# Performance work log

Hardware: AMD Instinct MI355X
Metric: run time of the kernel (lower is better)

The kernel has to match this reference:

```python
import jax, jax.numpy as jnp
import numpy as np

EMB, HEADS, DEPTH, SEQ, BATCH = 256, 8, 4, 8192, 4
DH = EMB // HEADS  # 32
FF = 4 * EMB
EPS = 1e-5


def setup_inputs() -> dict:
    key = jax.random.key(0)
    ks = jax.random.split(key, 8)
    w = lambda k, shape: jax.random.normal(k, shape, dtype=jnp.float32) * 0.02
    D = DEPTH
    return {
        "x": jax.random.normal(ks[0], (BATCH, SEQ, EMB), dtype=jnp.float32),
        "Wq": w(ks[1], (D, EMB, EMB)),
        "Wk": w(ks[2], (D, EMB, EMB)),
        "Wv": w(ks[3], (D, EMB, EMB)),
        "Wo": w(ks[4], (D, EMB, EMB)),
        "bo": jnp.zeros((D, EMB), jnp.float32),
        "ln1_g": jnp.ones((D, EMB), jnp.float32),
        "ln1_b": jnp.zeros((D, EMB), jnp.float32),
        "W1": w(ks[5], (D, EMB, FF)),
        "b1": jnp.zeros((D, FF), jnp.float32),
        "W2": w(ks[6], (D, FF, EMB)),
        "b2": jnp.zeros((D, EMB), jnp.float32),
        "ln2_g": jnp.ones((D, EMB), jnp.float32),
        "ln2_b": jnp.zeros((D, EMB), jnp.float32),
    }


def _layernorm(x, g, b):
    mu = x.mean(-1, keepdims=True)
    var = ((x - mu) ** 2).mean(-1, keepdims=True)
    return (x - mu) * jax.lax.rsqrt(var + EPS) * g + b


def _linear_attn(x, Wq, Wk, Wv, Wo, bo):
    # lucidrains linear_attn: q,k scaled by d**-0.25; softmax q over feature dim,
    # k over sequence dim; context = k^T v (per head), out = q @ context.
    b, n, dm = x.shape
    split = lambda t: t.reshape(b, n, HEADS, DH).transpose(0, 2, 1, 3)  # -> bhnd
    scale = DH ** -0.25
    q = jax.nn.softmax(split(x @ Wq) * scale, axis=-1)   # over d
    k = jax.nn.softmax(split(x @ Wk) * scale, axis=-2)   # over n
    v = split(x @ Wv)
    context = jnp.einsum('bhnd,bhne->bhde', k, v)        # [b,h,d,d]
    out = jnp.einsum('bhnd,bhde->bhne', q, context)      # [b,h,n,d]
    out = out.transpose(0, 2, 1, 3).reshape(b, n, dm)
    return out @ Wo + bo


def _forward(x, Wq, Wk, Wv, Wo, bo, ln1_g, ln1_b, W1, b1, W2, b2, ln2_g, ln2_b):
    for i in range(DEPTH):
        h = _layernorm(x, ln1_g[i], ln1_b[i])
        x = x + _linear_attn(h, Wq[i], Wk[i], Wv[i], Wo[i], bo[i])
        h = _layernorm(x, ln2_g[i], ln2_b[i])
        x = x + (jax.nn.gelu(h @ W1[i] + b1[i], approximate=False) @ W2[i] + b2[i])
    return x


def reference(x, Wq, Wk, Wv, Wo, bo, ln1_g, ln1_b, W1, b1, W2, b2, ln2_g, ln2_b):
    return _forward(x, Wq, Wk, Wv, Wo, bo, ln1_g, ln1_b, W1, b1, W2, b2, ln2_g, ln2_b)
```

## Files before the change

kernel.cpp:

```cpp
#include <hip/hip_runtime.h>
#include <hip/hip_bf16.h>

typedef __attribute__((ext_vector_type(8))) short bf16x8;
typedef __attribute__((ext_vector_type(4))) float f32x4;

#define EMB 256
#define HEADS 8
#define DH 32
#define SEQ 8192
#define BATCH 4
#define NROWS (SEQ*BATCH)
#define FFD 1024
#define DEPTH 4
#define QKVN 768
#define SCALE 0.42044820762685725f
#define NCHUNK 128
#define ROWS_PER_CHUNK (SEQ/NCHUNK)

static __device__ __forceinline__ float bf2f(ushort u){
  union { unsigned int i; float f; } x; x.i = ((unsigned int)u) << 16; return x.f;
}
static __device__ __forceinline__ ushort f2bf(float f){
  union { __hip_bfloat16 h; ushort u; } cv;
  cv.h = __float2bfloat16(f);
  return cv.u;
}
static __device__ __forceinline__ float gelu_f(float v){
  float y = 0.7978845608028654f * (v + 0.044715f*v*v*v);
  float e = __expf(2.0f*y);
  return 0.5f*v*(1.0f + (1.0f - 2.0f/(e + 1.0f)));
}

static __device__ __forceinline__ void gload_lds16(const ushort* g, ushort* l){
  __builtin_amdgcn_global_load_lds(
      (const __attribute__((address_space(1))) unsigned int*)(uintptr_t)g,
      (__attribute__((address_space(3))) unsigned int*)(uintptr_t)l,
      16, 0, 0);
}

__global__ __launch_bounds__(256) void prep_weights(
    const float* __restrict__ Wq, const float* __restrict__ Wk,
    const float* __restrict__ Wv, const float* __restrict__ Wo,
    const float* __restrict__ W1, const float* __restrict__ W2,
    ushort* __restrict__ wqkv_t, ushort* __restrict__ wo_t,
    ushort* __restrict__ w1_t, ushort* __restrict__ w2_t)
{
  __shared__ float tile[32][33];
  int bid = blockIdx.x;
  int L = bid / 768, r = bid % 768;
  const float* src; ushort* dst; int K, N, tidx;
  if (r < 192){ int which = r >> 6; tidx = r & 63;
    src = (which==0?Wq:which==1?Wk:Wv) + (long)L*65536;
    dst = wqkv_t + (long)L*QKVN*EMB + which*EMB*EMB; K=256; N=256;
  } else if (r < 256){ tidx = r-192; src = Wo + (long)L*65536; dst = wo_t + (long)L*65536; K=256; N=256; }
  else if (r < 512){ tidx = r-256; src = W1 + (long)L*262144; dst = w1_t + (long)L*262144; K=256; N=1024; }
  else { tidx = r-512; src = W2 + (long)L*262144; dst = w2_t + (long)L*262144; K=1024; N=256; }
  int tn = N >> 5;
  int tk = tidx / tn, tj = tidx % tn;
  int k0 = tk*32, n0 = tj*32;
  int c = threadIdx.x & 31, r0 = threadIdx.x >> 5;
  #pragma unroll
  for (int i=0;i<4;i++){
    int rr = r0 + i*8;
    tile[rr][c] = src[(long)(k0+rr)*N + n0 + c];
  }
  __syncthreads();
  #pragma unroll
  for (int i=0;i<4;i++){
    int rr = r0 + i*8;
    dst[(long)(n0+rr)*K + k0 + c] = f2bf(tile[c][rr]);
  }
}

__global__ __launch_bounds__(256) void ln_kernel(const float* __restrict__ x,
    const float* __restrict__ g, const float* __restrict__ bb,
    ushort* __restrict__ h)
{
  int wid = threadIdx.x >> 6, lane = threadIdx.x & 63;
  long row = (long)blockIdx.x*4 + wid;
  const float4 xv = *(const float4*)(x + row*EMB + lane*4);
  float s = xv.x+xv.y+xv.z+xv.w;
  float s2 = xv.x*xv.x+xv.y*xv.y+xv.z*xv.z+xv.w*xv.w;
  #pragma unroll
  for (int m=1;m<64;m<<=1){ s += __shfl_xor(s,m,64); s2 += __shfl_xor(s2,m,64); }
  float mean = s * (1.0f/EMB);
  float inv = rsqrtf(s2*(1.0f/EMB) - mean*mean + 1e-5f);
  float4 gv = *(const float4*)(g + lane*4);
  float4 bv = *(const float4*)(bb + lane*4);
  ushort4 o;
  o.x = f2bf((xv.x-mean)*inv*gv.x + bv.x);
  o.y = f2bf((xv.y-mean)*inv*gv.y + bv.y);
  o.z = f2bf((xv.z-mean)*inv*gv.z + bv.z);
  o.w = f2bf((xv.w-mean)*inv*gv.w + bv.w);
  *(ushort4*)(h + row*EMB + lane*4) = o;
}

template<int MODE, int BM, int BN, int BK>
__global__ __launch_bounds__(512, 2) void gemm_bt(
    const ushort* __restrict__ A, const ushort* __restrict__ Bt,
    int M, int N, int K,
    const float* __restrict__ bias,
    const float* __restrict__ xinf, const ushort* __restrict__ xinb,
    float* __restrict__ xoutf, ushort* __restrict__ xoutb,
    ushort* __restrict__ outb,
    const float* __restrict__ lng, const float* __restrict__ lnb)
{
  constexpr int NF = BN/64;
  constexpr int MR = BM/32;
  constexpr int MH = MR/4;
  constexpr int KK = BK/32;
  constexpr int CPR = BK/8;
  constexpr int AI = BM*BK/4096;
  constexpr int BI = BN*BK/4096;
  constexpr int TI = AI + BI;
  constexpr int NPH = KK*MH;
  __shared__ ushort LDSraw[2*BM*BK + 2*BN*BK];
  ushort* Abuf0 = LDSraw;
  ushort* Abuf1 = LDSraw + BM*BK;
  ushort* Bbuf0 = LDSraw + 2*BM*BK;
  ushort* Bbuf1 = LDSraw + 2*BM*BK + BN*BK;
  int t = threadIdx.x;
  int lane = t & 63, wid = t >> 6;
  int wr = wid >> 2, wc = wid & 3;
  int wrb = wr*(BM/2), wcb = wc*(BN/4);
  long rowA0 = (long)blockIdx.x * BM;
  long colB0 = (long)blockIdx.y * BN;
  const ushort* gA[AI]; int dA[AI];
  #pragma unroll
  for (int i=0;i<AI;i++){
    int l = i*512 + t;
    int row = l / CPR;
    int clog = (t % CPR) ^ (row & (CPR-1));
    gA[i] = A + (rowA0 + row)*(long)K + clog*8;
    dA[i] = l*8;
  }
  const ushort* gB[BI]; int dB[BI];
  #pragma unroll
  for (int i=0;i<BI;i++){
    int l = i*512 + t;
    int row = l / CPR;
    int clog = (t % CPR) ^ (row & (CPR-1));
    gB[i] = Bt + (colB0 + row)*(long)K + clog*8;
    dB[i] = l*8;
  }
  ushort* Ac = Abuf0; ushort* An = Abuf1;
  ushort* Bc = Bbuf0; ushort* Bn = Bbuf1;
  f32x4 acc[MR][NF] = {};
  int fr = lane & 15, cr4 = lane >> 4;
  int nsteps = K / BK;
  #pragma unroll
  for (int i=0;i<AI;i++) gload_lds16(gA[i], Ac + dA[i]);
  #pragma unroll
  for (int i=0;i<BI;i++) gload_lds16(gB[i], Bc + dB[i]);
  asm volatile("s_waitcnt vmcnt(0)" ::: "memory");
  __syncthreads();
  for (int s = 0; s < nsteps; ++s){
    bool pf = (s+1 < nsteps);
    long knext = (long)(s+1) * BK;
    #pragma unroll
    for (int kk=0; kk<KK; ++kk){
      int chunk = (((kk*4 + cr4)) ^ (fr & (CPR-1))) << 3;
      bf16x8 bv[NF];
      #pragma unroll
      for (int n=0;n<NF;n++)
        bv[n] = *(const bf16x8*)(Bc + (wcb + n*16 + fr)*BK + chunk);
      #pragma unroll
      for (int mh=0; mh<MH; ++mh){
        int sp = kk*MH + mh;
        bf16x8 av[4];
        #pragma unroll
        for (int m=0;m<4;m++)
          av[m] = *(const bf16x8*)(Ac + (wrb + (mh*4+m)*16 + fr)*BK + chunk);
        if (pf){
          #pragma unroll
          for (int j=0;j<TI;j++){
            if (j*NPH >= sp*TI && j*NPH < (sp+1)*TI){
              if (j < AI) gload_lds16(gA[j]+knext, An+dA[j]);
              else        gload_lds16(gB[j-AI]+knext, Bn+dB[j-AI]);
            }
          }
        }
        __builtin_amdgcn_s_setprio(1);
        #pragma unroll
        for (int m=0;m<4;m++){
          #pragma unroll
          for (int n=0;n<NF;n++)
            acc[mh*4+m][n] = __builtin_amdgcn_mfma_f32_16x16x32_bf16(av[m], bv[n], acc[mh*4+m][n], 0,0,0);
        }
        __builtin_amdgcn_s_setprio(0);
      }
    }
    asm volatile("s_waitcnt vmcnt(0)" ::: "memory");
    __syncthreads();
    ushort* tp;
    tp = Ac; Ac = An; An = tp;
    tp = Bc; Bc = Bn; Bn = tp;
  }
  constexpr int BNP = BN + 4;
  constexpr int ROUNDS = BM/32;
  constexpr int RPH = BM/64;
  float* bounce = (float*)LDSraw;
  int fq = lane >> 4;
  constexpr int TPR = BN/4;
  int rdrow = t / TPR;
  int rdcol = (t % TPR) * 4;
  constexpr int RPP = 512 / TPR;
  constexpr int PASSES = 32 / RPP;
  #pragma unroll
  for (int r = 0; r < ROUNDS; ++r){
    __syncthreads();
    if (wr == r / RPH){
      int mb = (r % RPH)*2;
      #pragma unroll
      for (int m4=0;m4<2;m4++){
        #pragma unroll
        for (int n=0;n<NF;n++){
          #pragma unroll
          for (int i=0;i<4;i++)
            bounce[(m4*16 + fq*4 + i)*BNP + wcb + n*16 + fr] = acc[mb+m4][n][i];
        }
      }
    }
    __syncthreads();
    long gr0 = rowA0 + r*32;
    #pragma unroll
    for (int p=0;p<PASSES;p++){
      int lr = p*RPP + rdrow;
      long gr = gr0 + lr;
      long gc = colB0 + rdcol;
      float4 v = *(float4*)&bounce[lr*BNP + rdcol];
      if (MODE==0){
        ushort4 o; o.x=f2bf(v.x); o.y=f2bf(v.y); o.z=f2bf(v.z); o.w=f2bf(v.w);
        *(ushort4*)&outb[gr*N + gc] = o;
      } else if (MODE==2){
        const float4 bv4 = *(const float4*)&bias[gc];
        ushort4 o;
        o.x = f2bf(gelu_f(v.x + bv4.x)); o.y = f2bf(gelu_f(v.y + bv4.y));
        o.z = f2bf(gelu_f(v.z + bv4.z)); o.w = f2bf(gelu_f(v.w + bv4.w));
        *(ushort4*)&outb[gr*N + gc] = o;
      } else {
        const float4 bv4 = *(const float4*)&bias[gc];
        float xo0, xo1, xo2, xo3;
        if (MODE==3){
          const float4 xo = *(const float4*)&xinf[gr*N + gc];
          xo0=xo.x; xo1=xo.y; xo2=xo.z; xo3=xo.w;
        } else {
          const ushort4 xb = *(const ushort4*)&xinb[gr*N + gc];
          xo0=bf2f(xb.x); xo1=bf2f(xb.y); xo2=bf2f(xb.z); xo3=bf2f(xb.w);
        }
        v.x += bv4.x + xo0; v.y += bv4.y + xo1;
        v.z += bv4.z + xo2; v.w += bv4.w + xo3;
        if (MODE==5){
          *(float4*)&xoutf[gr*N + gc] = v;
        } else {
          ushort4 xw;
          xw.x=f2bf(v.x); xw.y=f2bf(v.y); xw.z=f2bf(v.z); xw.w=f2bf(v.w);
          *(ushort4*)&xoutb[gr*N + gc] = xw;
          float s1 = v.x+v.y+v.z+v.w;
          float s2 = v.x*v.x+v.y*v.y+v.z*v.z+v.w*v.w;
          #pragma unroll
          for (int mm=1;mm<64;mm<<=1){ s1 += __shfl_xor(s1,mm,64); s2 += __shfl_xor(s2,mm,64); }
          float mean = s1 * (1.0f/EMB);
          float inv = rsqrtf(s2*(1.0f/EMB) - mean*mean + 1e-5f);
          const float4 g4 = *(const float4*)&lng[gc];
          const float4 b4 = *(const float4*)&lnb[gc];
          ushort4 o;
          o.x = f2bf((v.x-mean)*inv*g4.x + b4.x);
          o.y = f2bf((v.y-mean)*inv*g4.y + b4.y);
          o.z = f2bf((v.z-mean)*inv*g4.z + b4.z);
          o.w = f2bf((v.w-mean)*inv*g4.w + b4.w);
          *(ushort4*)&outb[gr*EMB + gc] = o;
        }
      }
    }
  }
}

__global__ __launch_bounds__(256) void colstats_partial(const ushort* __restrict__ qkv,
    float* __restrict__ pmax, float* __restrict__ psum)
{
  int ch = blockIdx.x, b = blockIdx.y;
  int t = threadIdx.x;
  const ushort* base = qkv + ((long)b*SEQ + (long)ch*ROWS_PER_CHUNK)*QKVN + EMB + t;
  float m[4] = {-1e30f,-1e30f,-1e30f,-1e30f};
  float s[4] = {0.f,0.f,0.f,0.f};
  #pragma unroll 2
  for (int n = 0; n < ROWS_PER_CHUNK; n += 4){
    #pragma unroll
    for (int j=0;j<4;j++){
      float v = bf2f(base[(long)(n+j)*QKVN]) * SCALE;
      float m2 = fmaxf(m[j], v);
      s[j] = s[j]*__expf(m[j]-m2) + __expf(v-m2);
      m[j] = m2;
    }
  }
  float M = fmaxf(fmaxf(m[0],m[1]), fmaxf(m[2],m[3]));
  float S = s[0]*__expf(m[0]-M) + s[1]*__expf(m[1]-M)
          + s[2]*__expf(m[2]-M) + s[3]*__expf(m[3]-M);
  long idx = ((long)b*NCHUNK + ch)*EMB + t;
  pmax[idx] = M; psum[idx] = S;
}

__global__ __launch_bounds__(256) void colstats_reduce(const float* __restrict__ pmax,
    const float* __restrict__ psum, float* __restrict__ kmax, float* __restrict__ ksum)
{
  int b = blockIdx.x, t = threadIdx.x;
  const float* pm = pmax + (long)b*NCHUNK*EMB + t;
  const float* ps = psum + (long)b*NCHUNK*EMB + t;
  float m = -1e30f, s = 0.f;
  for (int c = 0; c < NCHUNK; ++c){
    float cm = pm[(long)c*EMB], cs = ps[(long)c*EMB];
    float m2 = fmaxf(m, cm);
    s = s*__expf(m-m2) + cs*__expf(cm-m2);
    m = m2;
  }
  kmax[b*EMB + t] = m;
  ksum[b*EMB + t] = s;
}

__global__ __launch_bounds__(256) void ctx_partial(
    const ushort* __restrict__ qkv, const float* __restrict__ kmax,
    float* __restrict__ ctx_part)
{
  constexpr int LT = 72;
  __shared__ ushort ekT[32*LT];
  __shared__ ushort vvT[32*LT];
  int ch = blockIdx.x, h = blockIdx.y, b = blockIdx.z;
  int t = threadIdx.x, lane = t & 63, wid = t >> 6;
  long nbase = (long)b*SEQ + ch*512;
  int lrow = t >> 2, lseg = (t & 3) << 3;
  float km[8];
  #pragma unroll
  for (int j=0;j<8;j++) km[j] = kmax[b*256 + h*DH + lseg + j];
  int wstep = wid & 1, wdr = (wid >> 1) << 4;
  f32x4 acc0 = {}, acc1 = {};
  int frow = lane & 15, g8 = (lane >> 4) << 3;
  for (int st = 0; st < 8; ++st){
    long n0 = nbase + st*64;
    const ushort* gk = qkv + (n0 + lrow)*QKVN + EMB + h*DH + lseg;
    uint4 kv = *(const uint4*)gk;
    uint4 vv = *(const uint4*)(gk + EMB);
    __syncthreads();
    const ushort* kp = (const ushort*)&kv;
    const ushort* vp = (const ushort*)&vv;
    #pragma unroll
    for (int j=0;j<8;j++){
      float f = bf2f(kp[j])*SCALE;
      ekT[(lseg+j)*LT + lrow] = f2bf(__expf(f - km[j]));
      vvT[(lseg+j)*LT + lrow] = vp[j];
    }
    __syncthreads();
    bf16x8 afr = *(const bf16x8*)(ekT + (wdr + frow)*LT + wstep*32 + g8);
    bf16x8 bf0 = *(const bf16x8*)(vvT + frow*LT + wstep*32 + g8);
    bf16x8 bf1 = *(const bf16x8*)(vvT + (16 + frow)*LT + wstep*32 + g8);
    acc0 = __builtin_amdgcn_mfma_f32_16x16x32_bf16(afr, bf0, acc0, 0,0,0);
    acc1 = __builtin_amdgcn_mfma_f32_16x16x32_bf16(afr, bf1, acc1, 0,0,0);
  }
  int fq = lane >> 4;
  long pb = (((long)(b*HEADS+h))*32 + (ch*2+wstep))*1024;
  #pragma unroll
  for (int i=0;i<4;i++){
    ctx_part[pb + (wdr + fq*4 + i)*32 + frow] = acc0[i];
    ctx_part[pb + (wdr + fq*4 + i)*32 + 16 + frow] = acc1[i];
  }
}

__global__ __launch_bounds__(256) void ctx_reduce(const float* __restrict__ ctx_part,
    const float* __restrict__ ksum, ushort* __restrict__ ctxT)
{
  int bh = blockIdx.x; int b = bh >> 3, h = bh & 7;
  int t = threadIdx.x; int d = t >> 3, e4 = (t & 7) << 2;
  const float* p = ctx_part + (long)bh*32768 + d*32 + e4;
  float sx=0, sy=0, sz=0, sw=0;
  for (int c=0;c<32;c++){
    const float4 v = *(const float4*)(p + c*1024);
    sx+=v.x; sy+=v.y; sz+=v.z; sw+=v.w;
  }
  float inv = 1.0f / ksum[b*256 + h*DH + d];
  long base = (long)bh*1024;
  ctxT[base + (e4+0)*32 + d] = f2bf(sx*inv);
  ctxT[base + (e4+1)*32 + d] = f2bf(sy*inv);
  ctxT[base + (e4+2)*32 + d] = f2bf(sz*inv);
  ctxT[base + (e4+3)*32 + d] = f2bf(sw*inv);
}

__global__ __launch_bounds__(256) void attn_out(
    const ushort* __restrict__ qkv, const ushort* __restrict__ ctxT,
    ushort* __restrict__ ao)
{
  __shared__ ushort sq[4][16][264];
  int t = threadIdx.x, lane = t & 63, wid = t >> 6;
  long row0 = (long)blockIdx.x*64 + wid*16;
  int b = (int)(row0 / SEQ);
  int fr = lane & 15, g = lane >> 4;
  bf16x8 cf[8][2];
  #pragma unroll
  for (int h=0;h<8;h++){
    #pragma unroll
    for (int eh=0;eh<2;eh++)
      cf[h][eh] = *(const bf16x8*)(ctxT + ((long)(b*8+h)*32 + eh*16 + fr)*32 + g*8);
  }
  long gr = row0 + fr;
  #pragma unroll
  for (int hh=0;hh<2;hh++){
    int h = g*2 + hh;
    const ushort* qp = qkv + gr*QKVN + h*DH;
    union { uint4 v[4]; ushort u[32]; } qq;
    qq.v[0]=*(const uint4*)qp; qq.v[1]=*(const uint4*)(qp+8);
    qq.v[2]=*(const uint4*)(qp+16); qq.v[3]=*(const uint4*)(qp+24);
    float f[32]; float m = -1e30f;
    #pragma unroll
    for (int j=0;j<32;j++){ f[j] = bf2f(qq.u[j])*SCALE; m = fmaxf(m, f[j]); }
    float ssum = 0.f;
    #pragma unroll
    for (int j=0;j<32;j++){ f[j] = __expf(f[j]-m); ssum += f[j]; }
    float inv = 1.0f/ssum;
    union { uint4 v[4]; ushort u[32]; } oo;
    #pragma unroll
    for (int j=0;j<32;j++) oo.u[j] = f2bf(f[j]*inv);
    ushort* dst = &sq[wid][fr][h*DH];
    #pragma unroll
    for (int c2=0;c2<4;c2++) *(uint4*)(dst + c2*8) = oo.v[c2];
  }
  __syncthreads();
  #pragma unroll
  for (int h=0;h<8;h++){
    bf16x8 af = *(const bf16x8*)(&sq[wid][fr][h*DH + g*8]);
    f32x4 z = {};
    f32x4 o0 = __builtin_amdgcn_mfma_f32_16x16x32_bf16(af, cf[h][0], z, 0,0,0);
    f32x4 o1 = __builtin_amdgcn_mfma_f32_16x16x32_bf16(af, cf[h][1], z, 0,0,0);
    #pragma unroll
    for (int i=0;i<4;i++){
      long r = row0 + g*4 + i;
      ao[r*EMB + h*DH + fr]      = f2bf(o0[i]);
      ao[r*EMB + h*DH + 16 + fr] = f2bf(o1[i]);
    }
  }
}

extern "C" void kernel_launch(void* const* d_in, const int* in_sizes, int n_in,
                              void* d_out, int out_size, void* d_ws, size_t ws_size,
                              hipStream_t stream)
{
  const float* x_in = (const float*)d_in[0];
  const float* Wq  = (const float*)d_in[1];
  const float* Wk  = (const float*)d_in[2];
  const float* Wv  = (const float*)d_in[3];
  const float* Wo  = (const float*)d_in[4];
  const float* bo  = (const float*)d_in[5];
  const float* ln1g = (const float*)d_in[6];
  const float* ln1b = (const float*)d_in[7];
  const float* W1  = (const float*)d_in[8];
  const float* b1  = (const float*)d_in[9];
  const float* W2  = (const float*)d_in[10];
  const float* b2  = (const float*)d_in[11];
  const float* ln2g = (const float*)d_in[12];
  const float* ln2b = (const float*)d_in[13];
  float* xout = (float*)d_out;

  char* ws = (char*)d_ws;
  ushort* h_buf  = (ushort*)ws;  ws += (long)NROWS*EMB*2;
  ushort* xb     = (ushort*)ws;  ws += (long)NROWS*EMB*2;
  ushort* big    = (ushort*)ws;  ws += (long)NROWS*FFD*2;
  ushort* wqkv_t = (ushort*)ws;  ws += (long)DEPTH*QKVN*EMB*2;
  ushort* wo_t   = (ushort*)ws;  ws += (long)DEPTH*EMB*EMB*2;
  ushort* w1_t   = (ushort*)ws;  ws += (long)DEPTH*FFD*EMB*2;
  ushort* w2_t   = (ushort*)ws;  ws += (long)DEPTH*EMB*FFD*2;
  float*  kmax   = (float*)ws;   ws += (long)BATCH*EMB*4;
  float*  ksumv  = (float*)ws;   ws += (long)BATCH*EMB*4;
  float*  ctx_part = (float*)ws; ws += (long)BATCH*HEADS*32*1024*4;
  ushort* ctxT   = (ushort*)ws;  ws += (long)BATCH*HEADS*1024*2;
  float*  pmax   = (float*)ws;   ws += (long)BATCH*NCHUNK*EMB*4;
  float*  psum   = (float*)ws;   ws += (long)BATCH*NCHUNK*EMB*4;

  prep_weights<<<3072, 256, 0, stream>>>(Wq, Wk, Wv, Wo, W1, W2, wqkv_t, wo_t, w1_t, w2_t);
  ln_kernel<<<NROWS/4, 256, 0, stream>>>(x_in, ln1g, ln1b, h_buf);

  ushort* qkv = big;
  ushort* ffb = big;
  for (int L = 0; L < DEPTH; ++L){
    gemm_bt<0,128,128,64><<<dim3(NROWS/128, QKVN/128), 512, 0, stream>>>(
        h_buf, wqkv_t + (long)L*QKVN*EMB, NROWS, QKVN, EMB,
        nullptr, nullptr, nullptr, nullptr, nullptr, qkv, nullptr, nullptr);
    colstats_partial<<<dim3(NCHUNK, BATCH), 256, 0, stream>>>(qkv, pmax, psum);
    colstats_reduce<<<BATCH, 256, 0, stream>>>(pmax, psum, kmax, ksumv);
    ctx_partial<<<dim3(16, HEADS, BATCH), 256, 0, stream>>>(qkv, kmax, ctx_part);
    ctx_reduce<<<32, 256, 0, stream>>>(ctx_part, ksumv, ctxT);
    attn_out<<<NROWS/64, 256, 0, stream>>>(qkv, ctxT, h_buf);
    if (L == 0){
      gemm_bt<3,128,256,64><<<dim3(NROWS/128, 1), 512, 0, stream>>>(
          h_buf, wo_t, NROWS, EMB, EMB,
          bo, x_in, nullptr, nullptr, xb, h_buf, ln2g, ln2b);
    } else {
      gemm_bt<4,128,256,64><<<dim3(NROWS/128, 1), 512, 0, stream>>>(
          h_buf, wo_t + (long)L*EMB*EMB, NROWS, EMB, EMB,
          bo + L*EMB, nullptr, xb, nullptr, xb, h_buf,
          ln2g + L*EMB, ln2b + L*EMB);
    }
    gemm_bt<2,128,128,64><<<dim3(NROWS/128, FFD/128), 512, 0, stream>>>(
        h_buf, w1_t + (long)L*FFD*EMB, NROWS, FFD, EMB,
        b1 + L*FFD, nullptr, nullptr, nullptr, nullptr, ffb, nullptr, nullptr);
    if (L + 1 < DEPTH){
      gemm_bt<4,128,256,64><<<dim3(NROWS/128, 1), 512, 0, stream>>>(
          ffb, w2_t + (long)L*EMB*FFD, NROWS, EMB, FFD,
          b2 + L*EMB, nullptr, xb, nullptr, xb, h_buf,
          ln1g + (L+1)*EMB, ln1b + (L+1)*EMB);
    } else {
      gemm_bt<5,128,256,64><<<dim3(NROWS/128, 1), 512, 0, stream>>>(
          ffb, w2_t + (long)L*EMB*FFD, NROWS, EMB, FFD,
          b2 + L*EMB, nullptr, xb, xout, nullptr, nullptr, nullptr, nullptr);
    }
  }
}
```

Baseline: 630.0 us.

## Fuse FFN up-projection, GELU and down-projection into one kernel

Adds an ff_fused kernel. Each 512-thread block keeps a 128-row LayerNorm tile in LDS and loops over 64-wide slices of the 1024-wide hidden dimension. For each slice it computes the W1 product, applies bias and GELU into a shared tile, and accumulates the W2 product in registers. It then applies the residual, bias and the next LayerNorm in the epilogue. This removes the write and re-read of the 32768x1024 bf16 hidden activation and one launch per layer. In exchange it uses about 145KB of LDS, so only one block fits per CU, and the two GEMM phases within a block are serialised.

```diff
diff --git a/kernel.cpp b/kernel.cpp
--- a/kernel.cpp
+++ b/kernel.cpp
@@ -250,27 +250,197 @@
         }
         v.x += bv4.x + xo0; v.y += bv4.y + xo1;
         v.z += bv4.z + xo2; v.w += bv4.w + xo3;
-        if (MODE==5){
-          *(float4*)&xoutf[gr*N + gc] = v;
-        } else {
-          ushort4 xw;
-          xw.x=f2bf(v.x); xw.y=f2bf(v.y); xw.z=f2bf(v.z); xw.w=f2bf(v.w);
-          *(ushort4*)&xoutb[gr*N + gc] = xw;
-          float s1 = v.x+v.y+v.z+v.w;
-          float s2 = v.x*v.x+v.y*v.y+v.z*v.z+v.w*v.w;
+        ushort4 xw;
+        xw.x=f2bf(v.x); xw.y=f2bf(v.y); xw.z=f2bf(v.z); xw.w=f2bf(v.w);
+        *(ushort4*)&xoutb[gr*N + gc] = xw;
+        float s1 = v.x+v.y+v.z+v.w;
+        float s2 = v.x*v.x+v.y*v.y+v.z*v.z+v.w*v.w;
+        #pragma unroll
+        for (int mm=1;mm<64;mm<<=1){ s1 += __shfl_xor(s1,mm,64); s2 += __shfl_xor(s2,mm,64); }
+        float mean = s1 * (1.0f/EMB);
+        float inv = rsqrtf(s2*(1.0f/EMB) - mean*mean + 1e-5f);
+        const float4 g4 = *(const float4*)&lng[gc];
+        const float4 b4 = *(const float4*)&lnb[gc];
+        ushort4 o;
+        o.x = f2bf((v.x-mean)*inv*g4.x + b4.x);
+        o.y = f2bf((v.y-mean)*inv*g4.y + b4.y);
+        o.z = f2bf((v.z-mean)*inv*g4.z + b4.z);
+        o.w = f2bf((v.w-mean)*inv*g4.w + b4.w);
+        *(ushort4*)&outb[gr*EMB + gc] = o;
+      }
+    }
+  }
+}
+
+template<int MODE>
+__global__ __launch_bounds__(512) void ff_fused(
+    const ushort* __restrict__ A, const ushort* __restrict__ w1t,
+    const ushort* __restrict__ w2t,
+    const float* __restrict__ b1, const float* __restrict__ b2,
+    const ushort* __restrict__ xinb,
+    float* __restrict__ xoutf, ushort* __restrict__ xoutb,
+    ushort* __restrict__ hout,
+    const float* __restrict__ lng, const float* __restrict__ lnb)
+{
+  __shared__ ushort As[128*256];
+  __shared__ ushort W1b[64*256];
+  __shared__ ushort W2b[256*64];
+  __shared__ ushort Ps[128*68];
+  int t = threadIdx.x, lane = t & 63, wid = t >> 6;
+  int fr = lane & 15, cr4 = lane >> 4, fq = lane >> 4;
+  long rowA0 = (long)blockIdx.x * 128;
+  #pragma unroll
+  for (int i=0;i<8;i++){
+    int l = i*512 + t;
+    int row = l >> 5;
+    int clog = (l & 31) ^ (row & 31);
+    gload_lds16(A + (rowA0+row)*256 + clog*8, As + l*8);
+  }
+  #pragma unroll
+  for (int i=0;i<4;i++){
+    int l = i*512 + t;
+    int row = l >> 5;
+    int clog = (l & 31) ^ (row & 31);
+    gload_lds16(w1t + row*256 + clog*8, W1b + l*8);
+  }
+  asm volatile("s_waitcnt vmcnt(0)" ::: "memory");
+  __syncthreads();
+  int rwP = (wid & 3)*32, fwP = (wid >> 2)*32;
+  int rw2 = (wid >> 2)*64, cw2 = (wid & 3)*64;
+  f32x4 accC[4][4] = {};
+  for (int j = 0; j < 16; ++j){
+    f32x4 accP[2][2] = {};
+    #pragma unroll
+    for (int kk=0; kk<8; ++kk){
+      if ((kk & 1) == 0){
+        int i = kk >> 1;
+        int l = i*512 + t;
+        int row = l >> 3, c = l & 7;
+        int clog = c ^ (row & 7);
+        gload_lds16(w2t + row*1024 + j*64 + clog*8, W2b + l*8);
+      }
+      int ci = kk*4 + cr4;
+      bf16x8 av[2], wv[2];
+      #pragma unroll
+      for (int m=0;m<2;m++){
+        int row = rwP + m*16 + fr;
+        av[m] = *(const bf16x8*)(As + row*256 + ((ci ^ (row&31)) << 3));
+      }
+      #pragma unroll
+      for (int n=0;n<2;n++){
+        int row = fwP + n*16 + fr;
+        wv[n] = *(const bf16x8*)(W1b + row*256 + ((ci ^ (row&31)) << 3));
+      }
+      __builtin_amdgcn_s_setprio(1);
+      #pragma unroll
+      for (int m=0;m<2;m++){
+        #pragma unroll
+        for (int n=0;n<2;n++)
+          accP[m][n] = __builtin_amdgcn_mfma_f32_16x16x32_bf16(av[m], wv[n], accP[m][n], 0,0,0);
+      }
+      __builtin_amdgcn_s_setprio(0);
+    }
+    #pragma unroll
+    for (int n=0;n<2;n++){
+      float bv = b1[j*64 + fwP + n*16 + fr];
+      #pragma unroll
+      for (int m=0;m<2;m++){
+        #pragma unroll
+        for (int i2=0;i2<4;i2++){
+          int row = rwP + m*16 + fq*4 + i2;
+          Ps[row*68 + fwP + n*16 + fr] = f2bf(gelu_f(accP[m][n][i2] + bv));
+        }
+      }
+    }
+    asm volatile("s_waitcnt vmcnt(0)" ::: "memory");
+    __syncthreads();
+    bool pw1 = (j+1 < 16);
+    #pragma unroll
+    for (int kk2=0; kk2<2; ++kk2){
+      if (pw1){
+        #pragma unroll
+        for (int i=0;i<2;i++){
+          int ii = kk2*2 + i;
+          int l = ii*512 + t;
+          int row = l >> 5;
+          int clog = (l & 31) ^ (row & 31);
+          gload_lds16(w1t + (long)(j+1)*64*256 + row*256 + clog*8, W1b + l*8);
+        }
+      }
+      int ci2 = kk2*4 + cr4;
+      bf16x8 pv[4], wv2[4];
+      #pragma unroll
+      for (int m=0;m<4;m++){
+        int row = rw2 + m*16 + fr;
+        pv[m] = *(const bf16x8*)(Ps + row*68 + ci2*8);
+      }
+      #pragma unroll
+      for (int n=0;n<4;n++){
+        int row = cw2 + n*16 + fr;
+        wv2[n] = *(const bf16x8*)(W2b + row*64 + ((ci2 ^ (row&7)) << 3));
+      }
+      __builtin_amdgcn_s_setprio(1);
+      #pragma unroll
+      for (int m=0;m<4;m++){
+        #pragma unroll
+        for (int n=0;n<4;n++)
+          accC[m][n] = __builtin_amdgcn_mfma_f32_16x16x32_bf16(pv[m], wv2[n], accC[m][n], 0,0,0);
+      }
+      __builtin_amdgcn_s_setprio(0);
+    }
+    asm volatile("s_waitcnt vmcnt(0)" ::: "memory");
+    __syncthreads();
+  }
+  float* bounce = (float*)As;
+  int rdrow = t >> 6;
+  int rdcol = (t & 63) * 4;
+  #pragma unroll
+  for (int r = 0; r < 4; ++r){
+    __syncthreads();
+    if ((wid >> 2) == (r >> 1)){
+      int mb = (r & 1)*2;
+      #pragma unroll
+      for (int m4=0;m4<2;m4++){
+        #pragma unroll
+        for (int n=0;n<4;n++){
           #pragma unroll
-          for (int mm=1;mm<64;mm<<=1){ s1 += __shfl_xor(s1,mm,64); s2 += __shfl_xor(s2,mm,64); }
-          float mean = s1 * (1.0f/EMB);
-          float inv = rsqrtf(s2*(1.0f/EMB) - mean*mean + 1e-5f);
-          const float4 g4 = *(const float4*)&lng[gc];
-          const float4 b4 = *(const float4*)&lnb[gc];
-          ushort4 o;
-          o.x = f2bf((v.x-mean)*inv*g4.x + b4.x);
-          o.y = f2bf((v.y-mean)*inv*g4.y + b4.y);
-          o.z = f2bf((v.z-mean)*inv*g4.z + b4.z);
-          o.w = f2bf((v.w-mean)*inv*g4.w + b4.w);
-          *(ushort4*)&outb[gr*EMB + gc] = o;
+          for (int i2=0;i2<4;i2++)
+            bounce[(m4*16 + fq*4 + i2)*260 + cw2 + n*16 + fr] = accC[mb+m4][n][i2];
         }
+      }
+    }
+    __syncthreads();
+    long gr0 = rowA0 + r*32;
+    #pragma unroll
+    for (int p=0;p<4;p++){
+      int lr = p*8 + rdrow;
+      long gr = gr0 + lr;
+      long gc = rdcol;
+      float4 v = *(float4*)&bounce[lr*260 + rdcol];
+      const float4 bv4 = *(const float4*)&b2[gc];
+      const ushort4 xb4 = *(const ushort4*)&xinb[gr*EMB + gc];
+      v.x += bv4.x + bf2f(xb4.x); v.y += bv4.y + bf2f(xb4.y);
+      v.z += bv4.z + bf2f(xb4.z); v.w += bv4.w + bf2f(xb4.w);
+      if (MODE==5){
+        *(float4*)&xoutf[gr*EMB + gc] = v;
+      } else {
+        ushort4 xw;
+        xw.x=f2bf(v.x); xw.y=f2bf(v.y); xw.z=f2bf(v.z); xw.w=f2bf(v.w);
+        *(ushort4*)&xoutb[gr*EMB + gc] = xw;
+        float s1 = v.x+v.y+v.z+v.w;
+        float s2 = v.x*v.x+v.y*v.y+v.z*v.z+v.w*v.w;
+        #pragma unroll
+        for (int mm=1;mm<64;mm<<=1){ s1 += __shfl_xor(s1,mm,64); s2 += __shfl_xor(s2,mm,64); }
+        float mean = s1 * (1.0f/EMB);
+        float inv = rsqrtf(s2*(1.0f/EMB) - mean*mean + 1e-5f);
+        const float4 g4 = *(const float4*)&lng[gc];
+        const float4 b4 = *(const float4*)&lnb[gc];
+        ushort4 o;
+        o.x = f2bf((v.x-mean)*inv*g4.x + b4.x);
+        o.y = f2bf((v.y-mean)*inv*g4.y + b4.y);
+        o.z = f2bf((v.z-mean)*inv*g4.z + b4.z);
+        o.w = f2bf((v.w-mean)*inv*g4.w + b4.w);
+        *(ushort4*)&hout[gr*EMB + gc] = o;
       }
     }
   }
@@ -477,7 +647,6 @@
   ln_kernel<<<NROWS/4, 256, 0, stream>>>(x_in, ln1g, ln1b, h_buf);
 
   ushort* qkv = big;
-  ushort* ffb = big;
   for (int L = 0; L < DEPTH; ++L){
     gemm_bt<0,128,128,64><<<dim3(NROWS/128, QKVN/128), 512, 0, stream>>>(
         h_buf, wqkv_t + (long)L*QKVN*EMB, NROWS, QKVN, EMB,
@@ -497,18 +666,16 @@
           bo + L*EMB, nullptr, xb, nullptr, xb, h_buf,
           ln2g + L*EMB, ln2b + L*EMB);
     }
-    gemm_bt<2,128,128,64><<<dim3(NROWS/128, FFD/128), 512, 0, stream>>>(
-        h_buf, w1_t + (long)L*FFD*EMB, NROWS, FFD, EMB,
-        b1 + L*FFD, nullptr, nullptr, nullptr, nullptr, ffb, nullptr, nullptr);
     if (L + 1 < DEPTH){
-      gemm_bt<4,128,256,64><<<dim3(NROWS/128, 1), 512, 0, stream>>>(
-          ffb, w2_t + (long)L*EMB*FFD, NROWS, EMB, FFD,
-          b2 + L*EMB, nullptr, xb, nullptr, xb, h_buf,
+      ff_fused<4><<<256, 512, 0, stream>>>(
+          h_buf, w1_t + (long)L*FFD*EMB, w2_t + (long)L*EMB*FFD,
+          b1 + L*FFD, b2 + L*EMB, xb, nullptr, xb, h_buf,
           ln1g + (L+1)*EMB, ln1b + (L+1)*EMB);
     } else {
-      gemm_bt<5,128,256,64><<<dim3(NROWS/128, 1), 512, 0, stream>>>(
-          ffb, w2_t + (long)L*EMB*FFD, NROWS, EMB, FFD,
-          b2 + L*EMB, nullptr, xb, xout, nullptr, nullptr, nullptr, nullptr);
-    }
-  }
-}
+      ff_fused<5><<<256, 512, 0, stream>>>(
+          h_buf, w1_t + (long)L*FFD*EMB, w2_t + (long)L*EMB*FFD,
+          b1 + L*FFD, b2 + L*EMB, xb, xout, nullptr, nullptr,
+          nullptr, nullptr);
+    }
+  }
+}
```

New measurement: 582.8 us. -7.5%, faster.
